# Performance work log

Hardware: AMD Instinct MI355X
Metric: run time of the kernel (lower is better)

## Reference

```python
import jax, jax.numpy as jnp
import numpy as np

DS = 32   # self_obs_dim
DO = 32   # obstacle_obs_dim
D = DS + DO
H = 128   # obstacle_hidden_size
B = 512   # batch_size
A = 16    # num_adv_obs = 2 * num_oppo_obs


def _init_linear(key, fan_in, fan_out):
    kw, kb = jax.random.split(key)
    bound = 1.0 / np.sqrt(fan_in)
    w = jax.random.uniform(kw, (fan_in, fan_out), jnp.float32, -bound, bound)
    b = jax.random.uniform(kb, (fan_out,), jnp.float32, -bound, bound)
    return w, b


def setup_inputs() -> dict:
    key = jax.random.key(0)
    ks = jax.random.split(key, 10)
    obs = jax.random.normal(ks[0], (B, DS), jnp.float32)
    latent = jax.random.normal(ks[1], (B, A, DO), jnp.float32)
    hw1, hb1 = _init_linear(ks[2], D, H)
    hw2, hb2 = _init_linear(ks[3], H, D * H)
    vw1, vb1 = _init_linear(ks[4], H, H)
    vw2, vb2 = _init_linear(ks[5], H, H)
    aw1, ab1 = _init_linear(ks[6], 2 * H, H)
    aw2, ab2 = _init_linear(ks[7], H, H)
    aw3, ab3 = _init_linear(ks[8], H, 1)
    return {
        "obs": obs, "obs_intention_latent": latent,
        "hw1": hw1, "hb1": hb1, "hw2": hw2, "hb2": hb2,
        "vw1": vw1, "vb1": vb1, "vw2": vw2, "vb2": vb2,
        "aw1": aw1, "ab1": ab1, "aw2": aw2, "ab2": ab2,
        "aw3": aw3, "ab3": ab3,
        "num_adv_obs": A, "batch_size": B, "num_groups": 1,
    }


def reference(obs, obs_intention_latent, hw1, hb1, hw2, hb2,
              vw1, vb1, vw2, vb2, aw1, ab1, aw2, ab2, aw3, ab3,
              num_adv_obs, batch_size, num_groups):
    relu = jax.nn.relu
    # flatten opponents (batch-major, matches torch .reshape)
    obs_obstacles = obs_intention_latent.reshape(-1, DO)          # [N, DO]
    # torch .repeat(num_adv_obs, 1) tiles the batch dim
    self_rep = jnp.tile(obs[:, :DS], (num_adv_obs, 1))            # [N, DS]
    mlp_input = jnp.concatenate([self_rep, obs_obstacles], axis=1)  # [N, D]
    # hypernet: per-sample weight [N, D, H]
    h = relu(mlp_input @ hw1 + hb1)
    w = relu(h @ hw2 + hb2).reshape(-1, D, H)
    # per-sample vector-matrix product + tanh
    emb = jnp.tanh(jnp.einsum("nd,ndh->nh", mlp_input, w))        # [N, H]
    # neighbor value MLP
    vals = relu(relu(emb @ vw1 + vb1) @ vw2 + vb2)                # [N, H]
    # attention: concat with per-batch mean embedding
    emb_mean = jnp.mean(emb.reshape(batch_size, -1, H), axis=1)   # [B, H]
    mean_rep = jnp.tile(emb_mean, (num_adv_obs, 1))               # [N, H]
    att_in = jnp.concatenate([emb, mean_rep], axis=1)             # [N, 2H]
    scores = relu(relu(att_in @ aw1 + ab1) @ aw2 + ab2) @ aw3 + ab3  # [N, 1]
    att = jax.nn.softmax(scores.reshape(batch_size, -1), axis=1).reshape(-1, 1)
    weighted = (att * vals).reshape(batch_size, -1, H)
    return jnp.sum(weighted, axis=1)                              # [B, H]
```

## Files before the change

kernel.cpp:

```cpp
#include <hip/hip_runtime.h>
#include <hip/hip_bf16.h>
#include <math.h>

#define BATCH 512
#define NADV  16
#define NROWS (BATCH*NADV)
#define DS    32
#define DO    32
#define DIM   64
#define HID   128
#define WCOLS (DIM*HID)
#define LSTR  136

typedef _Float16 half8 __attribute__((ext_vector_type(8)));
typedef float floatx4 __attribute__((ext_vector_type(4)));

__global__ __launch_bounds__(256, 2)
void k_main(const float* __restrict__ obs, const float* __restrict__ latent,
            const float* __restrict__ hw1, const float* __restrict__ hb1,
            const float* __restrict__ hw2, const float* __restrict__ hb2,
            const float* __restrict__ vw1, const float* __restrict__ vw2,
            const float* __restrict__ aw1, const float* __restrict__ aw2,
            _Float16* __restrict__ embf, _Float16* __restrict__ emeanf,
            _Float16* __restrict__ vw1p, _Float16* __restrict__ vw2p,
            _Float16* __restrict__ aw1p, _Float16* __restrict__ aw2p) {
    __shared__ __align__(16) char smraw[71680];
    int b   = blockIdx.x;
    int tid = threadIdx.x;
    int wave = tid >> 6, lane = tid & 63, l15 = lane & 15, quad = lane >> 4;

    if (b >= 512) {
        float* smem = (float*)smraw;
        int u = b - 512;
        const float* src; _Float16* dst; int Kt, kt;
        if (u < 4)       { src = vw1; dst = vw1p; Kt = 4; kt = u; }
        else if (u < 8)  { src = vw2; dst = vw2p; Kt = 4; kt = u - 4; }
        else if (u < 16) { src = aw1; dst = aw1p; Kt = 8; kt = u - 8; }
        else             { src = aw2; dst = aw2p; Kt = 4; kt = u - 16; }
        for (int i = tid; i < 32 * 32; i += 256) {
            int r = i >> 5, c4 = (i & 31) * 4;
            *(float4*)&smem[r * 132 + c4] =
                *(const float4*)(src + (size_t)(kt * 32 + r) * HID + c4);
        }
        __syncthreads();
        for (int i = tid; i < 8 * 64; i += 256) {
            int ctl = i >> 6, ln = i & 63;
            int rbase = (ln >> 4) * 8, cc = ctl * 16 + (ln & 15);
            half8 v;
#pragma unroll
            for (int e = 0; e < 8; ++e) v[e] = (_Float16)smem[(rbase + e) * 132 + cc];
            *(half8*)(dst + ((size_t)ctl * Kt + kt) * 512 + ln * 8) = v;
        }
        return;
    }

    float (*xs_t)[132] = (float(*)[132])smraw;
    _Float16* hscr_all = (_Float16*)(smraw + 33792);
    _Float16 (*Bs)[2][4][512] = (_Float16(*)[2][4][512])(smraw + 33792);
    float* bias_s = (float*)(smraw + 67584);

    int jt = b & 7;
    int rt = b >> 3;
    int n0 = rt * 128;
    int j0 = jt * 16;

    for (int i = tid; i < 128 * 16; i += 256) {
        int r = i >> 4, c4 = (i & 15) * 4;
        float4 v;
        if (c4 < DS) v = *(const float4*)(obs + ((n0 + r) & (BATCH - 1)) * DS + c4);
        else         v = *(const float4*)(latent + (size_t)(n0 + r) * DO + (c4 - DS));
        xs_t[c4 + 0][r] = v.x;
        xs_t[c4 + 1][r] = v.y;
        xs_t[c4 + 2][r] = v.z;
        xs_t[c4 + 3][r] = v.w;
    }
    for (int i = tid; i < 64 * 16; i += 256)
        bias_s[i] = hb2[(i >> 4) * HID + j0 + (i & 15)];

    _Float16* hscr = hscr_all + wave * (32 * 132);
    half8 af[2][4];
    {
        half8 afx[2][2];
#pragma unroll
        for (int t = 0; t < 2; ++t) {
            int n = n0 + wave * 32 + t * 16 + l15;
            const float* orow = obs + (size_t)(n & (BATCH - 1)) * DS + quad * 8;
            const float* lrow = latent + (size_t)n * DO + quad * 8;
#pragma unroll
            for (int e = 0; e < 4; ++e) {
                afx[t][0][e]     = (_Float16)orow[e];
                afx[t][0][e + 4] = (_Float16)orow[e + 4];
                afx[t][1][e]     = (_Float16)lrow[e];
                afx[t][1][e + 4] = (_Float16)lrow[e + 4];
            }
        }
#pragma unroll
        for (int ct = 0; ct < 8; ++ct) {
            half8 bf[2];
#pragma unroll
            for (int ks = 0; ks < 2; ++ks) {
                const float* wsrc = hw1 + (size_t)(ks * 32 + quad * 8) * HID + ct * 16 + l15;
#pragma unroll
                for (int e = 0; e < 8; ++e) bf[ks][e] = (_Float16)wsrc[(size_t)e * HID];
            }
            float bb = hb1[ct * 16 + l15];
#pragma unroll
            for (int t = 0; t < 2; ++t) {
                floatx4 acc = {bb, bb, bb, bb};
#pragma unroll
                for (int ks = 0; ks < 2; ++ks)
                    acc = __builtin_amdgcn_mfma_f32_16x16x32_f16(afx[t][ks], bf[ks], acc, 0, 0, 0);
#pragma unroll
                for (int reg = 0; reg < 4; ++reg)
                    hscr[(t * 16 + quad * 4 + reg) * 132 + ct * 16 + l15] =
                        (_Float16)fmaxf(acc[reg], 0.f);
            }
        }
#pragma unroll
        for (int t = 0; t < 2; ++t)
#pragma unroll
            for (int ks = 0; ks < 4; ++ks)
                af[t][ks] = *(const half8*)&hscr[(t * 16 + l15) * 132 + ks * 32 + quad * 8];
    }
    __syncthreads();

    float emb_acc[2][4] = {{0.f, 0.f, 0.f, 0.f}, {0.f, 0.f, 0.f, 0.f}};

    {
        float g[16];
#pragma unroll
        for (int ci = 0; ci < 2; ++ci) {
            int c = wave * 2 + ci, dt = c >> 2, kt = c & 3;
            const float* src = hw2 + (size_t)(kt * 32 + quad * 8) * WCOLS
                                   + (size_t)dt * 128 + j0 + l15;
#pragma unroll
            for (int e = 0; e < 8; ++e) g[ci * 8 + e] = src[(size_t)e * WCOLS];
        }
#pragma unroll
        for (int ci = 0; ci < 2; ++ci) {
            int c = wave * 2 + ci, dt = c >> 2, kt = c & 3;
            half8 v;
#pragma unroll
            for (int e = 0; e < 8; ++e) v[e] = (_Float16)g[ci * 8 + e];
            *(half8*)&Bs[0][dt][kt][lane * 8] = v;
        }
    }
    __syncthreads();

    for (int it = 0; it < 32; ++it) {
        int cb = it & 1;
        bool have = (it < 31);
        float g[16];
        if (have) {
#pragma unroll
            for (int ci = 0; ci < 2; ++ci) {
                int c = wave * 2 + ci, dt = c >> 2, kt = c & 3;
                int d = (it + 1) * 2 + dt;
                const float* src = hw2 + (size_t)(kt * 32 + quad * 8) * WCOLS
                                       + (size_t)d * 128 + j0 + l15;
#pragma unroll
                for (int e = 0; e < 8; ++e) g[ci * 8 + e] = src[(size_t)e * WCOLS];
            }
        }
#pragma unroll
        for (int dd = 0; dd < 2; ++dd) {
            int d = it * 2 + dd;
            float bb = bias_s[d * 16 + l15];
            floatx4 acc0 = {bb, bb, bb, bb};
            floatx4 acc1 = {bb, bb, bb, bb};
#pragma unroll
            for (int ks = 0; ks < 4; ++ks) {
                half8 bfr = *(const half8*)&Bs[cb][dd][ks][lane * 8];
                acc0 = __builtin_amdgcn_mfma_f32_16x16x32_f16(af[0][ks], bfr, acc0, 0, 0, 0);
                acc1 = __builtin_amdgcn_mfma_f32_16x16x32_f16(af[1][ks], bfr, acc1, 0, 0, 0);
            }
            floatx4 xv0 = *(const floatx4*)&xs_t[d][wave * 32 + quad * 4];
            floatx4 xv1 = *(const floatx4*)&xs_t[d][wave * 32 + 16 + quad * 4];
#pragma unroll
            for (int reg = 0; reg < 4; ++reg) {
                emb_acc[0][reg] = fmaf(xv0[reg], fmaxf(acc0[reg], 0.f), emb_acc[0][reg]);
                emb_acc[1][reg] = fmaf(xv1[reg], fmaxf(acc1[reg], 0.f), emb_acc[1][reg]);
            }
        }
        if (have) {
#pragma unroll
            for (int ci = 0; ci < 2; ++ci) {
                int c = wave * 2 + ci, dt = c >> 2, kt = c & 3;
                half8 v;
#pragma unroll
                for (int e = 0; e < 8; ++e) v[e] = (_Float16)g[ci * 8 + e];
                *(half8*)&Bs[cb ^ 1][dt][kt][lane * 8] = v;
            }
        }
        __syncthreads();
    }

#pragma unroll
    for (int t = 0; t < 2; ++t) {
        float e[4];
#pragma unroll
        for (int reg = 0; reg < 4; ++reg) {
            e[reg] = tanhf(emb_acc[t][reg]);
            embf[(size_t)(n0 + wave * 32 + t * 16 + quad * 4 + reg) * HID + j0 + l15] =
                (_Float16)e[reg];
        }
        float s = e[0] + e[1] + e[2] + e[3];
        s += __shfl_xor(s, 16, 64);
        s += __shfl_xor(s, 32, 64);
        if (quad == 0)
            emeanf[(size_t)(rt * 8 + wave * 2 + t) * HID + j0 + l15] =
                (_Float16)(s * (1.f / 16));
    }
}

__global__ __launch_bounds__(512, 4)
void k_tail(const _Float16* __restrict__ embf, const _Float16* __restrict__ emeanf,
            const _Float16* __restrict__ vw1p, const float* __restrict__ vb1,
            const _Float16* __restrict__ vw2p, const float* __restrict__ vb2,
            const _Float16* __restrict__ aw1p, const float* __restrict__ ab1,
            const _Float16* __restrict__ aw2p, const float* __restrict__ ab2,
            const float* __restrict__ aw3, const float* __restrict__ ab3,
            float* __restrict__ out) {
    __shared__ _Float16 embs[16][LSTR];
    __shared__ _Float16 means[16][LSTR];
    __shared__ _Float16 tAs[16][LSTR];
    __shared__ _Float16 tBs[16][LSTR];
    __shared__ float scr[16][32];
    __shared__ float satt[16];
    __shared__ float att[16];
    int g = blockIdx.x;
    int n0 = g * 16;
    int tid = threadIdx.x;
    int wave = tid >> 6, lane = tid & 63, l15 = lane & 15, quad = lane >> 4;
    int ct = wave;

    {
        int m = tid >> 8, r = (tid >> 4) & 15, c8 = (tid & 15) * 8;
        if (m == 0)
            *(half8*)&embs[r][c8] = *(const half8*)(embf + (size_t)(n0 + r) * HID + c8);
        else
            *(half8*)&means[r][c8] =
                *(const half8*)(emeanf + (size_t)((n0 & 511) + r) * HID + c8);
    }
    __syncthreads();

    half8 av[4], amean[4];
#pragma unroll
    for (int ks = 0; ks < 4; ++ks) {
        av[ks]    = *(const half8*)&embs[l15][ks * 32 + quad * 8];
        amean[ks] = *(const half8*)&means[l15][ks * 32 + quad * 8];
    }

    floatx4 acc;
    {
        float bb = vb1[ct * 16 + l15];
        acc = (floatx4){bb, bb, bb, bb};
    }
#pragma unroll
    for (int ks = 0; ks < 4; ++ks) {
        half8 bfr = *(const half8*)(vw1p + ((size_t)ct * 4 + ks) * 512 + lane * 8);
        acc = __builtin_amdgcn_mfma_f32_16x16x32_f16(av[ks], bfr, acc, 0, 0, 0);
    }
#pragma unroll
    for (int reg = 0; reg < 4; ++reg)
        tAs[quad * 4 + reg][ct * 16 + l15] = (_Float16)fmaxf(acc[reg], 0.f);
    __syncthreads();

    half8 at[4];
#pragma unroll
    for (int ks = 0; ks < 4; ++ks)
        at[ks] = *(const half8*)&tAs[l15][ks * 32 + quad * 8];

    floatx4 vacc;
    {
        float bb = vb2[ct * 16 + l15];
        vacc = (floatx4){bb, bb, bb, bb};
    }
#pragma unroll
    for (int ks = 0; ks < 4; ++ks) {
        half8 bfr = *(const half8*)(vw2p + ((size_t)ct * 4 + ks) * 512 + lane * 8);
        vacc = __builtin_amdgcn_mfma_f32_16x16x32_f16(at[ks], bfr, vacc, 0, 0, 0);
    }

    floatx4 aacc;
    {
        float bb = ab1[ct * 16 + l15];
        aacc = (floatx4){bb, bb, bb, bb};
    }
#pragma unroll
    for (int ks = 0; ks < 8; ++ks) {
        half8 bfr = *(const half8*)(aw1p + ((size_t)ct * 8 + ks) * 512 + lane * 8);
        half8 a = (ks < 4) ? av[ks] : amean[ks - 4];
        aacc = __builtin_amdgcn_mfma_f32_16x16x32_f16(a, bfr, aacc, 0, 0, 0);
    }
#pragma unroll
    for (int reg = 0; reg < 4; ++reg)
        tBs[quad * 4 + reg][ct * 16 + l15] = (_Float16)fmaxf(aacc[reg], 0.f);
    __syncthreads();

    half8 aa[4];
#pragma unroll
    for (int ks = 0; ks < 4; ++ks)
        aa[ks] = *(const half8*)&tBs[l15][ks * 32 + quad * 8];

    floatx4 a2acc;
    {
        float bb = ab2[ct * 16 + l15];
        a2acc = (floatx4){bb, bb, bb, bb};
    }
#pragma unroll
    for (int ks = 0; ks < 4; ++ks) {
        half8 bfr = *(const half8*)(aw2p + ((size_t)ct * 4 + ks) * 512 + lane * 8);
        a2acc = __builtin_amdgcn_mfma_f32_16x16x32_f16(aa[ks], bfr, a2acc, 0, 0, 0);
    }
    __syncthreads();
#pragma unroll
    for (int reg = 0; reg < 4; ++reg)
        tAs[quad * 4 + reg][ct * 16 + l15] = (_Float16)fmaxf(a2acc[reg], 0.f);
    __syncthreads();

    {
        int r = tid >> 5, ch = tid & 31;
        float p = 0.f;
#pragma unroll
        for (int k = 0; k < 4; ++k)
            p += (float)tAs[r][ch * 4 + k] * aw3[ch * 4 + k];
        scr[r][ch] = p;
    }
    __syncthreads();
    if (tid < 16) {
        float s = ab3[0];
#pragma unroll
        for (int ch = 0; ch < 32; ++ch) s += scr[tid][ch];
        satt[tid] = s;
    }
    __syncthreads();
    if (tid < 16) {
        float m = -1e30f;
#pragma unroll
        for (int a = 0; a < 16; ++a) m = fmaxf(m, satt[a]);
        float S = 0.f;
#pragma unroll
        for (int a = 0; a < 16; ++a) S += expf(satt[a] - m);
        att[tid] = expf(satt[tid] - m) / S;
    }
    __syncthreads();

    {
        float p = 0.f;
#pragma unroll
        for (int reg = 0; reg < 4; ++reg)
            p += att[quad * 4 + reg] * fmaxf(vacc[reg], 0.f);
        p += __shfl_xor(p, 16, 64);
        p += __shfl_xor(p, 32, 64);
        if (quad == 0) out[(size_t)g * HID + ct * 16 + l15] = p;
    }
}

extern "C" void kernel_launch(void* const* d_in, const int* in_sizes, int n_in,
                              void* d_out, int out_size, void* d_ws, size_t ws_size,
                              hipStream_t stream) {
    const float* obs = (const float*)d_in[0];
    const float* lat = (const float*)d_in[1];
    const float* hw1 = (const float*)d_in[2];
    const float* hb1 = (const float*)d_in[3];
    const float* hw2 = (const float*)d_in[4];
    const float* hb2 = (const float*)d_in[5];
    const float* vw1 = (const float*)d_in[6];
    const float* vb1 = (const float*)d_in[7];
    const float* vw2 = (const float*)d_in[8];
    const float* vb2 = (const float*)d_in[9];
    const float* aw1 = (const float*)d_in[10];
    const float* ab1 = (const float*)d_in[11];
    const float* aw2 = (const float*)d_in[12];
    const float* ab2 = (const float*)d_in[13];
    const float* aw3 = (const float*)d_in[14];
    const float* ab3 = (const float*)d_in[15];
    float* out = (float*)d_out;

    char* ws = (char*)d_ws;
    _Float16*  embf   = (_Float16*)ws;  ws += (size_t)NROWS * HID * 2;
    _Float16*  emeanf = (_Float16*)ws;  ws += (size_t)BATCH * HID * 2;
    _Float16*  vw1p   = (_Float16*)ws;  ws += (size_t)HID * HID * 2;
    _Float16*  vw2p   = (_Float16*)ws;  ws += (size_t)HID * HID * 2;
    _Float16*  aw1p   = (_Float16*)ws;  ws += (size_t)2 * HID * HID * 2;
    _Float16*  aw2p   = (_Float16*)ws;  ws += (size_t)HID * HID * 2;

    hipLaunchKernelGGL(k_main, dim3(532), dim3(256), 0, stream,
                       obs, lat, hw1, hb1, hw2, hb2, vw1, vw2, aw1, aw2,
                       embf, emeanf, vw1p, vw2p, aw1p, aw2p);
    hipLaunchKernelGGL(k_tail, dim3(BATCH), dim3(512), 0, stream,
                       embf, emeanf, vw1p, vb1, vw2p, vb2,
                       aw1p, ab1, aw2p, ab2, aw3, ab3, out);
}
```

Before: 138.1 us.

## Pre-pack hypernet weight to fp16 and async-load it per wave with split-K

```diff
diff --git a/kernel.cpp b/kernel.cpp
--- a/kernel.cpp
+++ b/kernel.cpp
@@ -15,10 +15,38 @@
 typedef _Float16 half8 __attribute__((ext_vector_type(8)));
 typedef float floatx4 __attribute__((ext_vector_type(4)));
 
+__device__ inline void async_ld16(void* lds, const void* g) {
+    __builtin_amdgcn_global_load_lds(
+        (const __attribute__((address_space(1))) void*)g,
+        (__attribute__((address_space(3))) void*)lds, 16, 0, 0);
+}
+
+__global__ __launch_bounds__(256)
+void k_prep(const float* __restrict__ hw2, _Float16* __restrict__ w2p) {
+    __shared__ __align__(16) float smem[32 * 132];
+    int b = blockIdx.x, tid = threadIdx.x;
+    int jb = b >> 2, kt = b & 3;
+    for (int i = tid; i < 32 * 32; i += 256) {
+        int r = i >> 5, c4 = (i & 31) * 4;
+        *(float4*)&smem[r * 132 + c4] =
+            *(const float4*)(hw2 + (size_t)(kt * 32 + r) * WCOLS + jb * 128 + c4);
+    }
+    __syncthreads();
+    for (int i = tid; i < 8 * 64; i += 256) {
+        int ctl = i >> 6, ln = i & 63;
+        int ct = jb * 8 + ctl;
+        int rbase = (ln >> 4) * 8, cc = ctl * 16 + (ln & 15);
+        half8 v;
+#pragma unroll
+        for (int e = 0; e < 8; ++e) v[e] = (_Float16)smem[(rbase + e) * 132 + cc];
+        *(half8*)(w2p + ((size_t)ct * 4 + kt) * 512 + ln * 8) = v;
+    }
+}
+
 __global__ __launch_bounds__(256, 2)
 void k_main(const float* __restrict__ obs, const float* __restrict__ latent,
             const float* __restrict__ hw1, const float* __restrict__ hb1,
-            const float* __restrict__ hw2, const float* __restrict__ hb2,
+            const float* __restrict__ hb2, const _Float16* __restrict__ w2p,
             const float* __restrict__ vw1, const float* __restrict__ vw2,
             const float* __restrict__ aw1, const float* __restrict__ aw2,
             _Float16* __restrict__ embf, _Float16* __restrict__ emeanf,
@@ -55,7 +83,7 @@
     }
 
     float (*xs_t)[132] = (float(*)[132])smraw;
-    _Float16* hscr_all = (_Float16*)(smraw + 33792);
+    _Float16* hscr = (_Float16*)(smraw + 33792);
     _Float16 (*Bs)[2][4][512] = (_Float16(*)[2][4][512])(smraw + 33792);
     float* bias_s = (float*)(smraw + 67584);
 
@@ -77,8 +105,6 @@
     for (int i = tid; i < 64 * 16; i += 256)
         bias_s[i] = hb2[(i >> 4) * HID + j0 + (i & 15)];
 
-    _Float16* hscr = hscr_all + wave * (32 * 132);
-    half8 af[2][4];
     {
         half8 afx[2][2];
 #pragma unroll
@@ -87,11 +113,9 @@
             const float* orow = obs + (size_t)(n & (BATCH - 1)) * DS + quad * 8;
             const float* lrow = latent + (size_t)n * DO + quad * 8;
 #pragma unroll
-            for (int e = 0; e < 4; ++e) {
-                afx[t][0][e]     = (_Float16)orow[e];
-                afx[t][0][e + 4] = (_Float16)orow[e + 4];
-                afx[t][1][e]     = (_Float16)lrow[e];
-                afx[t][1][e + 4] = (_Float16)lrow[e + 4];
+            for (int e = 0; e < 8; ++e) {
+                afx[t][0][e] = (_Float16)orow[e];
+                afx[t][1][e] = (_Float16)lrow[e];
             }
         }
 #pragma unroll
@@ -112,104 +136,89 @@
                     acc = __builtin_amdgcn_mfma_f32_16x16x32_f16(afx[t][ks], bf[ks], acc, 0, 0, 0);
 #pragma unroll
                 for (int reg = 0; reg < 4; ++reg)
-                    hscr[(t * 16 + quad * 4 + reg) * 132 + ct * 16 + l15] =
+                    hscr[(wave * 32 + t * 16 + quad * 4 + reg) * 132 + ct * 16 + l15] =
                         (_Float16)fmaxf(acc[reg], 0.f);
             }
         }
-#pragma unroll
-        for (int t = 0; t < 2; ++t)
-#pragma unroll
-            for (int ks = 0; ks < 4; ++ks)
-                af[t][ks] = *(const half8*)&hscr[(t * 16 + l15) * 132 + ks * 32 + quad * 8];
-    }
-    __syncthreads();
-
-    float emb_acc[2][4] = {{0.f, 0.f, 0.f, 0.f}, {0.f, 0.f, 0.f, 0.f}};
-
-    {
-        float g[16];
-#pragma unroll
-        for (int ci = 0; ci < 2; ++ci) {
-            int c = wave * 2 + ci, dt = c >> 2, kt = c & 3;
-            const float* src = hw2 + (size_t)(kt * 32 + quad * 8) * WCOLS
-                                   + (size_t)dt * 128 + j0 + l15;
-#pragma unroll
-            for (int e = 0; e < 8; ++e) g[ci * 8 + e] = src[(size_t)e * WCOLS];
-        }
-#pragma unroll
-        for (int ci = 0; ci < 2; ++ci) {
-            int c = wave * 2 + ci, dt = c >> 2, kt = c & 3;
-            half8 v;
-#pragma unroll
-            for (int e = 0; e < 8; ++e) v[e] = (_Float16)g[ci * 8 + e];
-            *(half8*)&Bs[0][dt][kt][lane * 8] = v;
-        }
-    }
-    __syncthreads();
-
-    for (int it = 0; it < 32; ++it) {
-        int cb = it & 1;
-        bool have = (it < 31);
-        float g[16];
-        if (have) {
-#pragma unroll
-            for (int ci = 0; ci < 2; ++ci) {
-                int c = wave * 2 + ci, dt = c >> 2, kt = c & 3;
-                int d = (it + 1) * 2 + dt;
-                const float* src = hw2 + (size_t)(kt * 32 + quad * 8) * WCOLS
-                                       + (size_t)d * 128 + j0 + l15;
-#pragma unroll
-                for (int e = 0; e < 8; ++e) g[ci * 8 + e] = src[(size_t)e * WCOLS];
-            }
-        }
-#pragma unroll
-        for (int dd = 0; dd < 2; ++dd) {
-            int d = it * 2 + dd;
-            float bb = bias_s[d * 16 + l15];
-            floatx4 acc0 = {bb, bb, bb, bb};
-            floatx4 acc1 = {bb, bb, bb, bb};
-#pragma unroll
-            for (int ks = 0; ks < 4; ++ks) {
-                half8 bfr = *(const half8*)&Bs[cb][dd][ks][lane * 8];
-                acc0 = __builtin_amdgcn_mfma_f32_16x16x32_f16(af[0][ks], bfr, acc0, 0, 0, 0);
-                acc1 = __builtin_amdgcn_mfma_f32_16x16x32_f16(af[1][ks], bfr, acc1, 0, 0, 0);
-            }
-            floatx4 xv0 = *(const floatx4*)&xs_t[d][wave * 32 + quad * 4];
-            floatx4 xv1 = *(const floatx4*)&xs_t[d][wave * 32 + 16 + quad * 4];
-#pragma unroll
-            for (int reg = 0; reg < 4; ++reg) {
-                emb_acc[0][reg] = fmaf(xv0[reg], fmaxf(acc0[reg], 0.f), emb_acc[0][reg]);
-                emb_acc[1][reg] = fmaf(xv1[reg], fmaxf(acc1[reg], 0.f), emb_acc[1][reg]);
-            }
-        }
-        if (have) {
-#pragma unroll
-            for (int ci = 0; ci < 2; ++ci) {
-                int c = wave * 2 + ci, dt = c >> 2, kt = c & 3;
-                half8 v;
-#pragma unroll
-                for (int e = 0; e < 8; ++e) v[e] = (_Float16)g[ci * 8 + e];
-                *(half8*)&Bs[cb ^ 1][dt][kt][lane * 8] = v;
-            }
-        }
-        __syncthreads();
-    }
-
-#pragma unroll
-    for (int t = 0; t < 2; ++t) {
+    }
+    __syncthreads();
+
+    half8 af[8][4];
+#pragma unroll
+    for (int t = 0; t < 8; ++t)
+#pragma unroll
+        for (int ks = 0; ks < 4; ++ks)
+            af[t][ks] = *(const half8*)&hscr[(t * 16 + l15) * 132 + ks * 32 + quad * 8];
+    __syncthreads();
+
+    float emb_acc[8][4];
+#pragma unroll
+    for (int t = 0; t < 8; ++t)
+#pragma unroll
+        for (int reg = 0; reg < 4; ++reg) emb_acc[t][reg] = 0.f;
+
+    const _Float16* wsrc0 = w2p + (size_t)jt * 2048 + lane * 8;
+    auto STAGE = [&](int d, int buf) {
+        const _Float16* src = wsrc0 + (size_t)d * 16384;
+        _Float16* dst = &Bs[wave][buf][0][0];
+#pragma unroll
+        for (int kt = 0; kt < 4; ++kt)
+            async_ld16(dst + kt * 512, src + kt * 512);
+    };
+    STAGE(wave * 2, 0);
+    STAGE(wave * 2 + 1, 1);
+
+    for (int i = 0; i < 16; ++i) {
+        if (i < 15) asm volatile("s_waitcnt vmcnt(4)" ::: "memory");
+        else        asm volatile("s_waitcnt vmcnt(0)" ::: "memory");
+        __builtin_amdgcn_sched_barrier(0);
+        int d = (i >> 1) * 8 + wave * 2 + (i & 1);
+        int buf = i & 1;
+        half8 bfr0 = *(const half8*)&Bs[wave][buf][0][lane * 8];
+        half8 bfr1 = *(const half8*)&Bs[wave][buf][1][lane * 8];
+        half8 bfr2 = *(const half8*)&Bs[wave][buf][2][lane * 8];
+        half8 bfr3 = *(const half8*)&Bs[wave][buf][3][lane * 8];
+        float bb = bias_s[d * 16 + l15];
+#pragma unroll
+        for (int t = 0; t < 8; ++t) {
+            floatx4 acc = {bb, bb, bb, bb};
+            acc = __builtin_amdgcn_mfma_f32_16x16x32_f16(af[t][0], bfr0, acc, 0, 0, 0);
+            acc = __builtin_amdgcn_mfma_f32_16x16x32_f16(af[t][1], bfr1, acc, 0, 0, 0);
+            acc = __builtin_amdgcn_mfma_f32_16x16x32_f16(af[t][2], bfr2, acc, 0, 0, 0);
+            acc = __builtin_amdgcn_mfma_f32_16x16x32_f16(af[t][3], bfr3, acc, 0, 0, 0);
+            floatx4 xv = *(const floatx4*)&xs_t[d][t * 16 + quad * 4];
+#pragma unroll
+            for (int reg = 0; reg < 4; ++reg)
+                emb_acc[t][reg] = fmaf(xv[reg], fmaxf(acc[reg], 0.f), emb_acc[t][reg]);
+        }
+        if (i + 2 < 16) STAGE(d + 8, buf);
+    }
+    __syncthreads();
+
+    float* red = (float*)smraw;
+#pragma unroll
+    for (int t = 0; t < 8; ++t)
+#pragma unroll
+        for (int reg = 0; reg < 4; ++reg)
+            red[((wave * 128) + t * 16 + quad * 4 + reg) * 16 + l15] = emb_acc[t][reg];
+    __syncthreads();
+#pragma unroll
+    for (int t2 = 0; t2 < 2; ++t2) {
         float e[4];
 #pragma unroll
-        for (int reg = 0; reg < 4; ++reg) {
-            e[reg] = tanhf(emb_acc[t][reg]);
-            embf[(size_t)(n0 + wave * 32 + t * 16 + quad * 4 + reg) * HID + j0 + l15] =
-                (_Float16)e[reg];
-        }
-        float s = e[0] + e[1] + e[2] + e[3];
-        s += __shfl_xor(s, 16, 64);
-        s += __shfl_xor(s, 32, 64);
+        for (int rr = 0; rr < 4; ++rr) {
+            int row = wave * 32 + t2 * 16 + quad * 4 + rr;
+            float s = red[(0 * 128 + row) * 16 + l15] + red[(1 * 128 + row) * 16 + l15]
+                    + red[(2 * 128 + row) * 16 + l15] + red[(3 * 128 + row) * 16 + l15];
+            e[rr] = tanhf(s);
+            embf[(size_t)(n0 + row) * HID + j0 + l15] = (_Float16)e[rr];
+        }
+        float m = e[0] + e[1] + e[2] + e[3];
+        m += __shfl_xor(m, 16, 64);
+        m += __shfl_xor(m, 32, 64);
         if (quad == 0)
-            emeanf[(size_t)(rt * 8 + wave * 2 + t) * HID + j0 + l15] =
-                (_Float16)(s * (1.f / 16));
+            emeanf[(size_t)(rt * 8 + wave * 2 + t2) * HID + j0 + l15] =
+                (_Float16)(m * (1.f / 16));
     }
 }
 
@@ -380,14 +389,16 @@
 
     char* ws = (char*)d_ws;
     _Float16*  embf   = (_Float16*)ws;  ws += (size_t)NROWS * HID * 2;
+    _Float16*  w2p    = (_Float16*)ws;  ws += (size_t)WCOLS * HID * 2;
     _Float16*  emeanf = (_Float16*)ws;  ws += (size_t)BATCH * HID * 2;
     _Float16*  vw1p   = (_Float16*)ws;  ws += (size_t)HID * HID * 2;
     _Float16*  vw2p   = (_Float16*)ws;  ws += (size_t)HID * HID * 2;
     _Float16*  aw1p   = (_Float16*)ws;  ws += (size_t)2 * HID * HID * 2;
     _Float16*  aw2p   = (_Float16*)ws;  ws += (size_t)HID * HID * 2;
 
+    hipLaunchKernelGGL(k_prep, dim3(256), dim3(256), 0, stream, hw2, w2p);
     hipLaunchKernelGGL(k_main, dim3(532), dim3(256), 0, stream,
-                       obs, lat, hw1, hb1, hw2, hb2, vw1, vw2, aw1, aw2,
+                       obs, lat, hw1, hb1, hb2, w2p, vw1, vw2, aw1, aw2,
                        embf, emeanf, vw1p, vw2p, aw1p, aw2p);
     hipLaunchKernelGGL(k_tail, dim3(BATCH), dim3(512), 0, stream,
                        embf, emeanf, vw1p, vb1, vw2p, vb2,
```

After: 133.9 us. 1.03x faster.
